# Performance work log

Measured on AMD Instinct MI355X. Metric: run time of the kernel, lower is better.

## Reference

```python
import jax, jax.numpy as jnp
import numpy as np

N = 100000   # nodes
E = 1600000  # edges (avg degree 16)
H = 8        # heads
C = 64       # per-head channels
G = 64       # graphs in batch
IN = 3       # input channels
OUT = 10     # classes
NEG_SLOPE = 0.2  # PyG GATConv default


def setup_inputs() -> dict:
    key = jax.random.key(0)
    ks = jax.random.split(key, 16)
    s = 0.1
    return {
        "x": jax.random.normal(ks[0], (N, IN), jnp.float32),
        "edge_index": jax.random.randint(ks[1], (2, E), 0, N),
        "batch": jnp.sort(jax.random.randint(ks[2], (N,), 0, G)),
        "W1": jax.random.normal(ks[3], (IN, H * C), jnp.float32) * s,
        "a1s": jax.random.normal(ks[4], (H, C), jnp.float32) * s,
        "a1d": jax.random.normal(ks[5], (H, C), jnp.float32) * s,
        "b1": jnp.zeros((H * C,), jnp.float32),
        "W2": jax.random.normal(ks[6], (H * C, H * C), jnp.float32) * s,
        "a2s": jax.random.normal(ks[7], (H, C), jnp.float32) * s,
        "a2d": jax.random.normal(ks[8], (H, C), jnp.float32) * s,
        "b2": jnp.zeros((H * C,), jnp.float32),
        "Wc": jax.random.normal(ks[9], (H * C, OUT), jnp.float32) * s,
        "bc": jnp.zeros((OUT,), jnp.float32),
    }


def _gat_layer(x, W, a_s, a_d, b, src, dst, n):
    # h: [N, H, C] per-head projected features
    h = (x @ W).reshape(n, H, C)
    # per-node attention logits per head
    al_s = jnp.einsum('nhc,hc->nh', h, a_s)
    al_d = jnp.einsum('nhc,hc->nh', h, a_d)
    # per-edge raw scores, [E', H]
    e = jax.nn.leaky_relu(al_s[src] + al_d[dst], NEG_SLOPE)
    # segment softmax over incoming edges of each destination node
    m = jax.ops.segment_max(e, dst, num_segments=n)
    ex = jnp.exp(e - m[dst])
    den = jax.ops.segment_sum(ex, dst, num_segments=n)
    alpha = ex / den[dst]  # [E', H]
    # weighted scatter-aggregate of source messages
    out = jax.ops.segment_sum(alpha[:, :, None] * h[src], dst, num_segments=n)
    return out.reshape(n, H * C) + b


def reference(x, edge_index, batch, W1, a1s, a1d, b1, W2, a2s, a2d, b2, Wc, bc):
    n = x.shape[0]
    ar = jnp.arange(n)
    # PyG GATConv adds self-loops by default
    src = jnp.concatenate([edge_index[0], ar])
    dst = jnp.concatenate([edge_index[1], ar])

    x1 = jax.nn.elu(_gat_layer(x, W1, a1s, a1d, b1, src, dst, n))
    x2 = jax.nn.elu(_gat_layer(x1, W2, a2s, a2d, b2, src, dst, n))

    # global mean pool over graphs
    sums = jax.ops.segment_sum(x2, batch, num_segments=G)
    cnt = jax.ops.segment_sum(jnp.ones((n, 1), x2.dtype), batch, num_segments=G)
    pooled = sums / jnp.maximum(cnt, 1.0)
    return pooled @ Wc + bc
```

## Files before the change

### kernel.cpp

```cpp
#include <hip/hip_runtime.h>
#include <math.h>

#define N_NODES 100000
#define N_EDGES 1600000
#define EP (N_EDGES + N_NODES)
#define NH 8
#define NC 64
#define NG 64
#define HC 512
#define SCAN_BLOCKS ((N_NODES + 255) / 256)
#define NPART 32
#define BPSTR 80

typedef unsigned short bf16_t;
typedef unsigned char fp8_t;
typedef __attribute__((ext_vector_type(8))) short short8;
typedef __attribute__((ext_vector_type(4))) float floatx4;
typedef __attribute__((ext_vector_type(2))) float floatx2;

__device__ inline float bf2f(bf16_t u) {
    union { unsigned int i; float f; } x;
    x.i = (unsigned int)u << 16;
    return x.f;
}
__device__ inline bf16_t f2bf(float f) {
    union { float f; unsigned int i; } x;
    x.f = f;
    unsigned int b = x.i;
    return (bf16_t)((b + 0x7fffu + ((b >> 16) & 1u)) >> 16);
}
__device__ inline fp8_t f2fp8(float f) {
    int v = __builtin_amdgcn_cvt_pk_fp8_f32(f, f, 0, false);
    return (fp8_t)v;
}

__device__ inline void ldsload16(const void* g, void* l) {
    __builtin_amdgcn_global_load_lds(
        (const __attribute__((address_space(1))) unsigned int*)g,
        (__attribute__((address_space(3))) unsigned int*)l, 16, 0, 0);
}

#define NBW2T (HC * HC / 256)
__global__ void k_prepw2t(const float* __restrict__ W1, const float* __restrict__ a1s,
                          const float* __restrict__ a1d, float* __restrict__ wprep,
                          const float* __restrict__ W2, bf16_t* __restrict__ W2T) {
    if (blockIdx.x == NBW2T) {
        int t = threadIdx.x;
        if (t < 48) {
            int isD = t >= 24;
            int tt = t % 24;
            int h = tt / 3, k = tt % 3;
            const float* a = isD ? a1d : a1s;
            float s = 0.f;
            for (int c = 0; c < 64; c++) s += W1[k * HC + h * 64 + c] * a[h * 64 + c];
            wprep[t] = s;
        }
        return;
    }
    int i = blockIdx.x * 256 + threadIdx.x;
    int n = i >> 9, kp = i & 511;
    int k = (kp & 7) * 64 + (kp >> 3);
    W2T[i] = f2bf(W2[k * HC + n]);
}

__global__ void k_deg(const int* __restrict__ ei, int* __restrict__ deg) {
    int i = blockIdx.x * 256 + threadIdx.x;
    if (i >= EP) return;
    int d = (i < N_EDGES) ? ei[N_EDGES + i] : (i - N_EDGES);
    atomicAdd(&deg[d], 1);
}

__global__ void k_scan1(const int* __restrict__ deg, int* __restrict__ rowptr, int* __restrict__ part) {
    __shared__ int s[256];
    int t = threadIdx.x, i = blockIdx.x * 256 + t;
    int v = (i < N_NODES) ? deg[i] : 0;
    s[t] = v;
    __syncthreads();
    for (int off = 1; off < 256; off <<= 1) {
        int u = (t >= off) ? s[t - off] : 0;
        __syncthreads();
        s[t] += u;
        __syncthreads();
    }
    if (i < N_NODES) rowptr[i] = s[t] - v;
    if (t == 255) part[blockIdx.x] = s[t];
}

__global__ void k_scan2(int* __restrict__ part, int* __restrict__ rowptr, int* __restrict__ gstart) {
    __shared__ int s[512];
    int t = threadIdx.x;
    int v = (t < SCAN_BLOCKS) ? part[t] : 0;
    s[t] = v;
    __syncthreads();
    for (int off = 1; off < 512; off <<= 1) {
        int u = (t >= off) ? s[t - off] : 0;
        __syncthreads();
        s[t] += u;
        __syncthreads();
    }
    part[t] = s[t] - v;
    if (t == 0) rowptr[N_NODES] = EP;
    if (t <= NG) gstart[t] = N_NODES;
}

__global__ void k_scan3(const int* __restrict__ part, int* __restrict__ rowptr,
                        int* __restrict__ cursor, const float* __restrict__ x,
                        bf16_t* __restrict__ xb, const int* __restrict__ batch,
                        int* __restrict__ gstart) {
    int i = blockIdx.x * 256 + threadIdx.x;
    if (i < N_NODES) {
        int v = rowptr[i] + part[blockIdx.x];
        rowptr[i] = v;
        cursor[i] = v;
        ushort4 p;
        p.x = f2bf(x[i * 3 + 0]);
        p.y = f2bf(x[i * 3 + 1]);
        p.z = f2bf(x[i * 3 + 2]);
        p.w = 0;
        *(ushort4*)&xb[i * 4] = p;
        int b = batch[i];
        if (i == 0) {
            for (int g = 0; g <= b; g++) gstart[g] = 0;
        } else {
            int bp = batch[i - 1];
            if (b != bp)
                for (int g = bp + 1; g <= b; g++) gstart[g] = i;
        }
    }
}

__global__ void k_scatter(const int* __restrict__ ei, int* __restrict__ cursor, int* __restrict__ csr) {
    int i = blockIdx.x * 256 + threadIdx.x;
    if (i >= EP) return;
    int s, d;
    if (i < N_EDGES) { s = ei[i]; d = ei[N_EDGES + i]; }
    else { s = i - N_EDGES; d = s; }
    int pos = atomicAdd(&cursor[d], 1);
    csr[pos] = s;
}

__global__ __launch_bounds__(64) void k_layer1(
    const bf16_t* __restrict__ xb, const int* __restrict__ rowptr, const int* __restrict__ csr,
    const float* __restrict__ W1, const float* __restrict__ wprep, const float* __restrict__ b1,
    bf16_t* __restrict__ x1p) {
    __shared__ float w1s[1536];
    __shared__ float wp[48];
    int lane = threadIdx.x;
#pragma unroll
    for (int q = 0; q < 6; q++)
        *(float4*)&w1s[(q * 64 + lane) * 4] = *(const float4*)&W1[(q * 64 + lane) * 4];
    if (lane < 48) wp[lane] = wprep[lane];
    __syncthreads();
    int half = lane >> 5, l32 = lane & 31;
    int dst = blockIdx.x * 2 + half;
    int rs = rowptr[dst], re = rowptr[dst + 1];
    ushort4 xd4 = *(const ushort4*)&xb[dst * 4];
    float xdx = bf2f(xd4.x), xdy = bf2f(xd4.y), xdz = bf2f(xd4.z);
    float ald[NH];
#pragma unroll
    for (int h = 0; h < NH; h++)
        ald[h] = xdx * wp[24 + h * 3] + xdy * wp[24 + h * 3 + 1] + xdz * wp[24 + h * 3 + 2];
    float den[NH], c0[NH], c1[NH], c2[NH];
#pragma unroll
    for (int h = 0; h < NH; h++) { den[h] = 0.f; c0[h] = 0.f; c1[h] = 0.f; c2[h] = 0.f; }
    for (int base = rs; base < re; base += 32) {
        int e = base + l32;
        if (e < re) {
            int s = csr[e];
            ushort4 sv4 = *(const ushort4*)&xb[s * 4];
            float svx = bf2f(sv4.x), svy = bf2f(sv4.y), svz = bf2f(sv4.z);
#pragma unroll
            for (int h = 0; h < NH; h++) {
                float ev = svx * wp[h * 3] + svy * wp[h * 3 + 1] + svz * wp[h * 3 + 2] + ald[h];
                ev = fmaxf(ev, 0.2f * ev);
                float w = __expf(ev);
                den[h] += w;
                c0[h] += w * svx;
                c1[h] += w * svy;
                c2[h] += w * svz;
            }
        }
    }
#pragma unroll
    for (int h = 0; h < NH; h++) {
#pragma unroll
        for (int off = 1; off < 32; off <<= 1) {
            den[h] += __shfl_xor(den[h], off, 64);
            c0[h] += __shfl_xor(c0[h], off, 64);
            c1[h] += __shfl_xor(c1[h], off, 64);
            c2[h] += __shfl_xor(c2[h], off, 64);
        }
    }
    bf16_t vbA[NH], vbB[NH];
#pragma unroll
    for (int h = 0; h < NH; h++) {
        int colA = h * 64 + l32;
        float vA = c0[h] * w1s[colA] + c1[h] * w1s[512 + colA] + c2[h] * w1s[1024 + colA];
        vA = vA / den[h] + b1[colA];
        vA = vA > 0.f ? vA : (__expf(vA) - 1.f);
        vbA[h] = f2bf(vA);
        int colB = colA + 32;
        float vB = c0[h] * w1s[colB] + c1[h] * w1s[512 + colB] + c2[h] * w1s[1024 + colB];
        vB = vB / den[h] + b1[colB];
        vB = vB > 0.f ? vB : (__expf(vB) - 1.f);
        vbB[h] = f2bf(vB);
    }
    uint4 oA, oB;
    oA.x = (unsigned int)vbA[0] | ((unsigned int)vbA[1] << 16);
    oA.y = (unsigned int)vbA[2] | ((unsigned int)vbA[3] << 16);
    oA.z = (unsigned int)vbA[4] | ((unsigned int)vbA[5] << 16);
    oA.w = (unsigned int)vbA[6] | ((unsigned int)vbA[7] << 16);
    oB.x = (unsigned int)vbB[0] | ((unsigned int)vbB[1] << 16);
    oB.y = (unsigned int)vbB[2] | ((unsigned int)vbB[3] << 16);
    oB.z = (unsigned int)vbB[4] | ((unsigned int)vbB[5] << 16);
    oB.w = (unsigned int)vbB[6] | ((unsigned int)vbB[7] << 16);
    *(uint4*)&x1p[(size_t)dst * HC + l32 * 8] = oA;
    *(uint4*)&x1p[(size_t)dst * HC + (l32 + 32) * 8] = oB;
}

__global__ __launch_bounds__(256) void k_gemm2(const bf16_t* __restrict__ A,
                                               const bf16_t* __restrict__ BT,
                                               fp8_t* __restrict__ Out,
                                               int row_base, int nrows,
                                               const float* __restrict__ a2s,
                                               const float* __restrict__ a2d,
                                               float* __restrict__ al2s,
                                               float* __restrict__ al2d) {
    __shared__ short smem[16384];
    short* As = smem;
    short* Bs = smem + 8192;
    int tid = threadIdx.x;
    int lane = tid & 63, wave = tid >> 6;
    int wm = wave & 1, wn = wave >> 1;
    int lm = lane & 15, quad = lane >> 4;
    int gx = blockIdx.x, gy = blockIdx.y;
    int l8 = lane >> 3, lc8 = lane & 7;
    int sw = lc8 ^ l8;
    const bf16_t* ga[4];
    const bf16_t* gb[4];
    short* la[4];
    short* lb[4];
#pragma unroll
    for (int it = 0; it < 4; it++) {
        int ar = gy * 128 + wave * 32 + it * 8 + l8;
        int arc = (ar < nrows) ? ar : 0;
        ga[it] = A + (size_t)(row_base + arc) * HC + sw * 8;
        gb[it] = BT + (size_t)(gx * 128 + wave * 32 + it * 8 + l8) * HC + sw * 8;
        la[it] = As + (wave * 32 + it * 8) * 64;
        lb[it] = Bs + (wave * 32 + it * 8) * 64;
    }

    floatx4 acc[4][4];
#pragma unroll
    for (int mi = 0; mi < 4; mi++)
#pragma unroll
        for (int ni = 0; ni < 4; ni++) acc[mi][ni] = (floatx4){0.f, 0.f, 0.f, 0.f};

    int lmw = lm & 7;
    for (int k0 = 0; k0 < HC; k0 += 64) {
        __syncthreads();
#pragma unroll
        for (int it = 0; it < 4; it++) ldsload16(ga[it] + k0, la[it]);
#pragma unroll
        for (int it = 0; it < 4; it++) ldsload16(gb[it] + k0, lb[it]);
        __syncthreads();
        short8 af[4][2], bf[4][2];
#pragma unroll
        for (int mi = 0; mi < 4; mi++)
#pragma unroll
            for (int kk = 0; kk < 2; kk++) {
                int pos = (kk * 4 + quad) ^ lmw;
                af[mi][kk] = *(const short8*)&As[(wm * 64 + mi * 16 + lm) * 64 + pos * 8];
            }
#pragma unroll
        for (int ni = 0; ni < 4; ni++)
#pragma unroll
            for (int kk = 0; kk < 2; kk++) {
                int pos = (kk * 4 + quad) ^ lmw;
                bf[ni][kk] = *(const short8*)&Bs[(wn * 64 + ni * 16 + lm) * 64 + pos * 8];
            }
#pragma unroll
        for (int mi = 0; mi < 4; mi++)
#pragma unroll
            for (int ni = 0; ni < 4; ni++) {
                acc[mi][ni] = __builtin_amdgcn_mfma_f32_16x16x32_bf16(af[mi][0], bf[ni][0], acc[mi][ni], 0, 0, 0);
                acc[mi][ni] = __builtin_amdgcn_mfma_f32_16x16x32_bf16(af[mi][1], bf[ni][1], acc[mi][ni], 0, 0, 0);
            }
    }
    int head = gx * 2 + wn;
    float a2sv[4], a2dv[4];
#pragma unroll
    for (int ni = 0; ni < 4; ni++) {
        int col = gx * 128 + wn * 64 + ni * 16 + lm;
        a2sv[ni] = a2s[col];
        a2dv[ni] = a2d[col];
    }
#pragma unroll
    for (int mi = 0; mi < 4; mi++) {
#pragma unroll
        for (int rg = 0; rg < 4; rg++) {
            int lrow = gy * 128 + wm * 64 + mi * 16 + quad * 4 + rg;
            float ps = 0.f, pd = 0.f;
#pragma unroll
            for (int ni = 0; ni < 4; ni++) {
                float v = acc[mi][ni][rg];
                ps += v * a2sv[ni];
                pd += v * a2dv[ni];
            }
#pragma unroll
            for (int off = 1; off < 16; off <<= 1) {
                ps += __shfl_xor(ps, off, 64);
                pd += __shfl_xor(pd, off, 64);
            }
            if (lrow < nrows && lm == 0) {
                int ar = row_base + lrow;
                al2s[ar * NH + head] = ps;
                al2d[ar * NH + head] = pd;
            }
        }
    }
    __syncthreads();
    unsigned char* bpatch = (unsigned char*)smem + wave * (32 * BPSTR);
#pragma unroll
    for (int p = 0; p < 2; p++) {
#pragma unroll
        for (int mih = 0; mih < 2; mih++) {
            int mi = p * 2 + mih;
#pragma unroll
            for (int ni = 0; ni < 4; ni++)
#pragma unroll
                for (int rg = 0; rg < 4; rg++) {
                    int rl = mih * 16 + quad * 4 + rg;
                    bpatch[rl * BPSTR + ni * 16 + lm] = f2fp8(acc[mi][ni][rg]);
                }
        }
#pragma unroll
        for (int it = 0; it < 2; it++) {
            int idx = it * 64 + lane;
            int rl = idx >> 2, c16 = idx & 3;
            uint4 v = *(uint4*)&bpatch[rl * BPSTR + c16 * 16];
            int lrow = gy * 128 + wm * 64 + p * 32 + rl;
            if (lrow < nrows)
                *(uint4*)&Out[(size_t)lrow * HC + wn * 64 + gx * 128 + c16 * 16] = v;
        }
        __syncthreads();
    }
}

#define ACC8(v, w) do { floatx2 c_;                                                            \
    c_ = __builtin_amdgcn_cvt_pk_f32_fp8((v).x, false); acc[0] += (w) * c_.x; acc[1] += (w) * c_.y; \
    c_ = __builtin_amdgcn_cvt_pk_f32_fp8((v).x, true);  acc[2] += (w) * c_.x; acc[3] += (w) * c_.y; \
    c_ = __builtin_amdgcn_cvt_pk_f32_fp8((v).y, false); acc[4] += (w) * c_.x; acc[5] += (w) * c_.y; \
    c_ = __builtin_amdgcn_cvt_pk_f32_fp8((v).y, true);  acc[6] += (w) * c_.x; acc[7] += (w) * c_.y; \
} while (0)

__global__ __launch_bounds__(64) void k_layer2pool(
    const fp8_t* __restrict__ h2lo, const fp8_t* __restrict__ h2hi, int srows,
    const float* __restrict__ al2s, const float* __restrict__ al2d,
    const int* __restrict__ rowptr, const int* __restrict__ csr, const float* __restrict__ b2,
    const int* __restrict__ batch, float* __restrict__ poolpart) {
    __shared__ float wlds[528];
    __shared__ int slds[64];
    int lane = threadIdx.x;
    int hme = lane >> 3;
    int hb = hme * 65;
    int dst = blockIdx.x;
    int rs = rowptr[dst], re = rowptr[dst + 1];
    float4 d0 = *(const float4*)&al2d[dst * NH];
    float4 d1 = *(const float4*)&al2d[dst * NH + 4];
    float ald[NH] = {d0.x, d0.y, d0.z, d0.w, d1.x, d1.y, d1.z, d1.w};
    float den[NH], acc[8];
#pragma unroll
    for (int h = 0; h < NH; h++) den[h] = 0.f;
#pragma unroll
    for (int q = 0; q < 8; q++) acc[q] = 0.f;
    for (int base = rs; base < re; base += 64) {
        int e = base + lane;
        int cl = re - base; if (cl > 64) cl = 64;
        float w[NH];
        int s = 0;
        if (e < re) {
            s = csr[e];
            float4 p0 = *(const float4*)&al2s[s * NH];
            float4 p1 = *(const float4*)&al2s[s * NH + 4];
            float als[NH] = {p0.x, p0.y, p0.z, p0.w, p1.x, p1.y, p1.z, p1.w};
#pragma unroll
            for (int h = 0; h < NH; h++) {
                float ev = als[h] + ald[h];
                ev = fmaxf(ev, 0.2f * ev);
                w[h] = __expf(ev);
                den[h] += w[h];
            }
        } else {
#pragma unroll
            for (int h = 0; h < NH; h++) w[h] = 0.f;
        }
        slds[lane] = s;
#pragma unroll
        for (int h = 0; h < NH; h++) wlds[h * 65 + lane] = w[h];
        int j = 0;
        for (; j + 7 < cl; j += 8) {
            uint2 vv[8]; float ww[8];
#pragma unroll
            for (int u = 0; u < 8; u++) {
                int s0 = slds[j + u];
                ww[u] = wlds[hb + j + u];
                const fp8_t* bp = (s0 < srows) ? (h2lo + (size_t)s0 * HC)
                                               : (h2hi + (size_t)(s0 - srows) * HC);
                vv[u] = *(const uint2*)&bp[lane * 8];
            }
#pragma unroll
            for (int u = 0; u < 8; u++) ACC8(vv[u], ww[u]);
        }
        if (j + 3 < cl) {
            uint2 vv[4]; float ww[4];
#pragma unroll
            for (int u = 0; u < 4; u++) {
                int s0 = slds[j + u];
                ww[u] = wlds[hb + j + u];
                const fp8_t* bp = (s0 < srows) ? (h2lo + (size_t)s0 * HC)
                                               : (h2hi + (size_t)(s0 - srows) * HC);
                vv[u] = *(const uint2*)&bp[lane * 8];
            }
#pragma unroll
            for (int u = 0; u < 4; u++) ACC8(vv[u], ww[u]);
            j += 4;
        }
        for (; j < cl; j++) {
            int sA = slds[j];
            float wA = wlds[hb + j];
            const fp8_t* bA = (sA < srows) ? (h2lo + (size_t)sA * HC)
                                           : (h2hi + (size_t)(sA - srows) * HC);
            uint2 vA = *(const uint2*)&bA[lane * 8];
            ACC8(vA, wA);
        }
    }
#pragma unroll
    for (int h = 0; h < NH; h++)
#pragma unroll
        for (int off = 1; off < 64; off <<= 1) den[h] += __shfl_xor(den[h], off, 64);
    float dd = den[0];
#pragma unroll
    for (int h = 1; h < NH; h++) dd = (hme == h) ? den[h] : dd;
    float dinv = 1.0f / dd;
    float4 ba = *(const float4*)&b2[lane * 8];
    float4 bb = *(const float4*)&b2[lane * 8 + 4];
    float bv[8] = {ba.x, ba.y, ba.z, ba.w, bb.x, bb.y, bb.z, bb.w};
#pragma unroll
    for (int q = 0; q < 8; q++) {
        float v = acc[q] * dinv + bv[q];
        v = v > 0.f ? v : (__expf(v) - 1.f);
        int c = lane * 8 + q;
        wlds[c + (c >> 5)] = v;
    }
    int g = batch[dst];
    float* pp = poolpart + ((size_t)(blockIdx.x & (NPART - 1)) * NG + g) * HC;
#pragma unroll
    for (int h = 0; h < NH; h++) {
        int c = h * 64 + lane;
        atomicAdd(&pp[c], wlds[c + (c >> 5)]);
    }
}

__global__ __launch_bounds__(256) void k_poolcls(const float* __restrict__ poolpart,
                                                 const int* __restrict__ gstart,
                                                 const float* __restrict__ Wc,
                                                 const float* __restrict__ bc,
                                                 float* __restrict__ out) {
    __shared__ float pl[512];
    int g = blockIdx.x, t = threadIdx.x;
    for (int c = t; c < HC; c += 256) {
        float s = 0.f;
        for (int p = 0; p < NPART; p++) s += poolpart[(size_t)p * NG * HC + g * HC + c];
        pl[c] = s;
    }
    __syncthreads();
    if (t < 10) {
        float cnt = fmaxf((float)(gstart[g + 1] - gstart[g]), 1.0f);
        float acc = 0.f;
        for (int k = 0; k < HC; k++) acc += pl[k] * Wc[k * 10 + t];
        out[g * 10 + t] = acc / cnt + bc[t];
    }
}

extern "C" void kernel_launch(void* const* d_in, const int* in_sizes, int n_in,
                              void* d_out, int out_size, void* d_ws, size_t ws_size,
                              hipStream_t stream) {
    const float* x   = (const float*)d_in[0];
    const int*   ei  = (const int*)d_in[1];
    const int*   bat = (const int*)d_in[2];
    const float* W1  = (const float*)d_in[3];
    const float* a1s = (const float*)d_in[4];
    const float* a1d = (const float*)d_in[5];
    const float* b1  = (const float*)d_in[6];
    const float* W2  = (const float*)d_in[7];
    const float* a2s = (const float*)d_in[8];
    const float* a2d = (const float*)d_in[9];
    const float* b2  = (const float*)d_in[10];
    const float* Wc  = (const float*)d_in[11];
    const float* bc  = (const float*)d_in[12];
    float* out = (float*)d_out;

    char* ws = (char*)d_ws;
    size_t off = 0;
    auto alloc = [&](size_t bytes) {
        size_t o = off;
        off += (bytes + 255) & ~(size_t)255;
        return o;
    };
    float*  wprep    = (float*)(ws + alloc(48 * 4));
    int*    rowptr   = (int*)(ws + alloc((size_t)(N_NODES + 1) * 4));
    int*    deg      = (int*)(ws + alloc((size_t)N_NODES * 4));
    int*    cursor   = (int*)(ws + alloc((size_t)N_NODES * 4));
    int*    part     = (int*)(ws + alloc(512 * 4));
    int*    gstart   = (int*)(ws + alloc(65 * 4));
    bf16_t* xb       = (bf16_t*)(ws + alloc((size_t)N_NODES * 4 * 2));
    int*    csr      = (int*)(ws + alloc((size_t)EP * 4));
    bf16_t* x1b      = (bf16_t*)(ws + alloc((size_t)N_NODES * HC * 2));
    float*  al2s     = (float*)(ws + alloc((size_t)N_NODES * NH * 4));
    float*  al2d     = (float*)(ws + alloc((size_t)N_NODES * NH * 4));
    float*  poolpart = (float*)(ws + alloc((size_t)NPART * NG * HC * 4));
    bf16_t* W2T = (bf16_t*)deg;

    size_t rem = (ws_size > off) ? ws_size - off : 0;
    int nslices, srows;
    if (rem >= (size_t)N_NODES * HC)      { nslices = 1;  srows = N_NODES; }
    else if (rem >= (size_t)50000 * HC)   { nslices = 2;  srows = 50000; }
    else if (rem >= (size_t)25000 * HC)   { nslices = 4;  srows = 25000; }
    else if (rem >= (size_t)12500 * HC)   { nslices = 8;  srows = 12500; }
    else                                  { nslices = 16; srows = 6250; }
    fp8_t* T = (fp8_t*)(ws + alloc((size_t)srows * HC));
    fp8_t* h2hi = (fp8_t*)x1b;

    hipMemsetAsync(deg, 0, (size_t)N_NODES * 4, stream);
    hipMemsetAsync(poolpart, 0, (size_t)NPART * NG * HC * 4, stream);

    k_deg<<<(EP + 255) / 256, 256, 0, stream>>>(ei, deg);
    k_scan1<<<SCAN_BLOCKS, 256, 0, stream>>>(deg, rowptr, part);
    k_scan2<<<1, 512, 0, stream>>>(part, rowptr, gstart);
    k_scan3<<<SCAN_BLOCKS, 256, 0, stream>>>(part, rowptr, cursor, x, xb, bat, gstart);
    k_scatter<<<(EP + 255) / 256, 256, 0, stream>>>(ei, cursor, csr);
    k_prepw2t<<<NBW2T + 1, 256, 0, stream>>>(W1, a1s, a1d, wprep, W2, W2T);
    k_layer1<<<N_NODES / 2, 64, 0, stream>>>(xb, rowptr, csr, W1, wprep, b1, x1b);
    for (int s = 0; s < nslices; s++) {
        fp8_t* outp = (s == 0) ? T : (h2hi + (size_t)(s - 1) * srows * HC);
        k_gemm2<<<dim3(4, (srows + 127) / 128), 256, 0, stream>>>(
            x1b, W2T, outp, s * srows, srows, a2s, a2d, al2s, al2d);
    }
    k_layer2pool<<<N_NODES, 64, 0, stream>>>(T, h2hi, srows, al2s, al2d,
                                             rowptr, csr, b2, bat, poolpart);
    k_poolcls<<<NG, 256, 0, stream>>>(poolpart, gstart, Wc, bc, out);
}
```

Baseline: 725.2 us.

## Process 16 destinations per block and pre-reduce pooling in LDS

The layer-2 aggregation+pool kernel now runs 256-thread blocks that each handle 16 consecutive destination nodes, four per wave. Because batch is sorted, each block's nodes map to at most a couple of graphs, so per-node outputs are summed in shared memory and flushed to global poolpart once per block rather than once per node. This cuts global atomic traffic by roughly 16x and reduces block launch count, at the cost of LDS atomics and a serial 4-node loop per wave that may lengthen tail latency on high-degree nodes.

```diff
diff --git a/kernel.cpp b/kernel.cpp
--- a/kernel.cpp
+++ b/kernel.cpp
@@ -11,6 +11,7 @@
 #define SCAN_BLOCKS ((N_NODES + 255) / 256)
 #define NPART 32
 #define BPSTR 80
+#define DPB 16
 
 typedef unsigned short bf16_t;
 typedef unsigned char fp8_t;
@@ -354,111 +355,136 @@
     c_ = __builtin_amdgcn_cvt_pk_f32_fp8((v).y, true);  acc[6] += (w) * c_.x; acc[7] += (w) * c_.y; \
 } while (0)
 
-__global__ __launch_bounds__(64) void k_layer2pool(
+__global__ __launch_bounds__(256) void k_layer2pool(
     const fp8_t* __restrict__ h2lo, const fp8_t* __restrict__ h2hi, int srows,
     const float* __restrict__ al2s, const float* __restrict__ al2d,
     const int* __restrict__ rowptr, const int* __restrict__ csr, const float* __restrict__ b2,
     const int* __restrict__ batch, float* __restrict__ poolpart) {
-    __shared__ float wlds[528];
-    __shared__ int slds[64];
-    int lane = threadIdx.x;
+    __shared__ float pacc[2][528];
+    __shared__ float wlds[4][528];
+    __shared__ int slds[4][64];
+    int tid = threadIdx.x;
+    int wave = tid >> 6, lane = tid & 63;
+    int base = blockIdx.x * DPB;
+    for (int c = tid; c < 1056; c += 256) ((float*)pacc)[c] = 0.f;
+    int g0 = batch[base];
+    int g1 = batch[base + DPB - 1];
+    __syncthreads();
     int hme = lane >> 3;
     int hb = hme * 65;
-    int dst = blockIdx.x;
-    int rs = rowptr[dst], re = rowptr[dst + 1];
-    float4 d0 = *(const float4*)&al2d[dst * NH];
-    float4 d1 = *(const float4*)&al2d[dst * NH + 4];
-    float ald[NH] = {d0.x, d0.y, d0.z, d0.w, d1.x, d1.y, d1.z, d1.w};
-    float den[NH], acc[8];
-#pragma unroll
-    for (int h = 0; h < NH; h++) den[h] = 0.f;
-#pragma unroll
-    for (int q = 0; q < 8; q++) acc[q] = 0.f;
-    for (int base = rs; base < re; base += 64) {
-        int e = base + lane;
-        int cl = re - base; if (cl > 64) cl = 64;
-        float w[NH];
-        int s = 0;
-        if (e < re) {
-            s = csr[e];
-            float4 p0 = *(const float4*)&al2s[s * NH];
-            float4 p1 = *(const float4*)&al2s[s * NH + 4];
-            float als[NH] = {p0.x, p0.y, p0.z, p0.w, p1.x, p1.y, p1.z, p1.w};
-#pragma unroll
-            for (int h = 0; h < NH; h++) {
-                float ev = als[h] + ald[h];
-                ev = fmaxf(ev, 0.2f * ev);
-                w[h] = __expf(ev);
-                den[h] += w[h];
-            }
-        } else {
-#pragma unroll
-            for (int h = 0; h < NH; h++) w[h] = 0.f;
-        }
-        slds[lane] = s;
-#pragma unroll
-        for (int h = 0; h < NH; h++) wlds[h * 65 + lane] = w[h];
-        int j = 0;
-        for (; j + 7 < cl; j += 8) {
-            uint2 vv[8]; float ww[8];
-#pragma unroll
-            for (int u = 0; u < 8; u++) {
-                int s0 = slds[j + u];
-                ww[u] = wlds[hb + j + u];
-                const fp8_t* bp = (s0 < srows) ? (h2lo + (size_t)s0 * HC)
-                                               : (h2hi + (size_t)(s0 - srows) * HC);
-                vv[u] = *(const uint2*)&bp[lane * 8];
-            }
-#pragma unroll
-            for (int u = 0; u < 8; u++) ACC8(vv[u], ww[u]);
-        }
-        if (j + 3 < cl) {
-            uint2 vv[4]; float ww[4];
-#pragma unroll
-            for (int u = 0; u < 4; u++) {
-                int s0 = slds[j + u];
-                ww[u] = wlds[hb + j + u];
-                const fp8_t* bp = (s0 < srows) ? (h2lo + (size_t)s0 * HC)
-                                               : (h2hi + (size_t)(s0 - srows) * HC);
-                vv[u] = *(const uint2*)&bp[lane * 8];
-            }
-#pragma unroll
-            for (int u = 0; u < 4; u++) ACC8(vv[u], ww[u]);
-            j += 4;
-        }
-        for (; j < cl; j++) {
-            int sA = slds[j];
-            float wA = wlds[hb + j];
-            const fp8_t* bA = (sA < srows) ? (h2lo + (size_t)sA * HC)
-                                           : (h2hi + (size_t)(sA - srows) * HC);
-            uint2 vA = *(const uint2*)&bA[lane * 8];
-            ACC8(vA, wA);
-        }
-    }
-#pragma unroll
-    for (int h = 0; h < NH; h++)
-#pragma unroll
-        for (int off = 1; off < 64; off <<= 1) den[h] += __shfl_xor(den[h], off, 64);
-    float dd = den[0];
-#pragma unroll
-    for (int h = 1; h < NH; h++) dd = (hme == h) ? den[h] : dd;
-    float dinv = 1.0f / dd;
     float4 ba = *(const float4*)&b2[lane * 8];
     float4 bb = *(const float4*)&b2[lane * 8 + 4];
     float bv[8] = {ba.x, ba.y, ba.z, ba.w, bb.x, bb.y, bb.z, bb.w};
-#pragma unroll
-    for (int q = 0; q < 8; q++) {
-        float v = acc[q] * dinv + bv[q];
-        v = v > 0.f ? v : (__expf(v) - 1.f);
-        int c = lane * 8 + q;
-        wlds[c + (c >> 5)] = v;
-    }
-    int g = batch[dst];
-    float* pp = poolpart + ((size_t)(blockIdx.x & (NPART - 1)) * NG + g) * HC;
-#pragma unroll
-    for (int h = 0; h < NH; h++) {
-        int c = h * 64 + lane;
-        atomicAdd(&pp[c], wlds[c + (c >> 5)]);
+    float* mywlds = wlds[wave];
+    int* myslds = slds[wave];
+    for (int di = 0; di < 4; di++) {
+        int dst = base + wave * 4 + di;
+        int rs = rowptr[dst], re = rowptr[dst + 1];
+        float4 d0 = *(const float4*)&al2d[dst * NH];
+        float4 d1 = *(const float4*)&al2d[dst * NH + 4];
+        float ald[NH] = {d0.x, d0.y, d0.z, d0.w, d1.x, d1.y, d1.z, d1.w};
+        float den[NH], acc[8];
+#pragma unroll
+        for (int h = 0; h < NH; h++) den[h] = 0.f;
+#pragma unroll
+        for (int q = 0; q < 8; q++) acc[q] = 0.f;
+        for (int eb = rs; eb < re; eb += 64) {
+            int e = eb + lane;
+            int cl = re - eb; if (cl > 64) cl = 64;
+            float w[NH];
+            int s = 0;
+            if (e < re) {
+                s = csr[e];
+                float4 p0 = *(const float4*)&al2s[s * NH];
+                float4 p1 = *(const float4*)&al2s[s * NH + 4];
+                float als[NH] = {p0.x, p0.y, p0.z, p0.w, p1.x, p1.y, p1.z, p1.w};
+#pragma unroll
+                for (int h = 0; h < NH; h++) {
+                    float ev = als[h] + ald[h];
+                    ev = fmaxf(ev, 0.2f * ev);
+                    w[h] = __expf(ev);
+                    den[h] += w[h];
+                }
+            } else {
+#pragma unroll
+                for (int h = 0; h < NH; h++) w[h] = 0.f;
+            }
+            myslds[lane] = s;
+#pragma unroll
+            for (int h = 0; h < NH; h++) mywlds[h * 65 + lane] = w[h];
+            int j = 0;
+            for (; j + 7 < cl; j += 8) {
+                uint2 vv[8]; float ww[8];
+#pragma unroll
+                for (int u = 0; u < 8; u++) {
+                    int s0 = myslds[j + u];
+                    ww[u] = mywlds[hb + j + u];
+                    const fp8_t* bp = (s0 < srows) ? (h2lo + (size_t)s0 * HC)
+                                                   : (h2hi + (size_t)(s0 - srows) * HC);
+                    vv[u] = *(const uint2*)&bp[lane * 8];
+                }
+#pragma unroll
+                for (int u = 0; u < 8; u++) ACC8(vv[u], ww[u]);
+            }
+            if (j + 3 < cl) {
+                uint2 vv[4]; float ww[4];
+#pragma unroll
+                for (int u = 0; u < 4; u++) {
+                    int s0 = myslds[j + u];
+                    ww[u] = mywlds[hb + j + u];
+                    const fp8_t* bp = (s0 < srows) ? (h2lo + (size_t)s0 * HC)
+                                                   : (h2hi + (size_t)(s0 - srows) * HC);
+                    vv[u] = *(const uint2*)&bp[lane * 8];
+                }
+#pragma unroll
+                for (int u = 0; u < 4; u++) ACC8(vv[u], ww[u]);
+                j += 4;
+            }
+            for (; j < cl; j++) {
+                int sA = myslds[j];
+                float wA = mywlds[hb + j];
+                const fp8_t* bA = (sA < srows) ? (h2lo + (size_t)sA * HC)
+                                               : (h2hi + (size_t)(sA - srows) * HC);
+                uint2 vA = *(const uint2*)&bA[lane * 8];
+                ACC8(vA, wA);
+            }
+        }
+#pragma unroll
+        for (int h = 0; h < NH; h++)
+#pragma unroll
+            for (int off = 1; off < 64; off <<= 1) den[h] += __shfl_xor(den[h], off, 64);
+        float dd = den[0];
+#pragma unroll
+        for (int h = 1; h < NH; h++) dd = (hme == h) ? den[h] : dd;
+        float dinv = 1.0f / dd;
+        int g = batch[dst];
+        if (g == g0 || g == g1) {
+            float* pa = pacc[(g == g0) ? 0 : 1];
+#pragma unroll
+            for (int q = 0; q < 8; q++) {
+                float v = acc[q] * dinv + bv[q];
+                v = v > 0.f ? v : (__expf(v) - 1.f);
+                int c = lane * 8 + q;
+                atomicAdd(&pa[c + (c >> 5)], v);
+            }
+        } else {
+            float* pp = poolpart + ((size_t)(blockIdx.x & (NPART - 1)) * NG + g) * HC;
+#pragma unroll
+            for (int q = 0; q < 8; q++) {
+                float v = acc[q] * dinv + bv[q];
+                v = v > 0.f ? v : (__expf(v) - 1.f);
+                atomicAdd(&pp[lane * 8 + q], v);
+            }
+        }
+    }
+    __syncthreads();
+    float* pp0 = poolpart + ((size_t)(blockIdx.x & (NPART - 1)) * NG + g0) * HC;
+    for (int c = tid; c < HC; c += 256)
+        atomicAdd(&pp0[c], pacc[0][c + (c >> 5)]);
+    if (g1 != g0) {
+        float* pp1 = poolpart + ((size_t)(blockIdx.x & (NPART - 1)) * NG + g1) * HC;
+        for (int c = tid; c < HC; c += 256)
+            atomicAdd(&pp1[c], pacc[1][c + (c >> 5)]);
     }
 }
 
@@ -547,7 +573,7 @@
         k_gemm2<<<dim3(4, (srows + 127) / 128), 256, 0, stream>>>(
             x1b, W2T, outp, s * srows, srows, a2s, a2d, al2s, al2d);
     }
-    k_layer2pool<<<N_NODES, 64, 0, stream>>>(T, h2hi, srows, al2s, al2d,
-                                             rowptr, csr, b2, bat, poolpart);
+    k_layer2pool<<<N_NODES / DPB, 256, 0, stream>>>(T, h2hi, srows, al2s, al2d,
+                                                    rowptr, csr, b2, bat, poolpart);
     k_poolcls<<<NG, 256, 0, stream>>>(poolpart, gstart, Wc, bc, out);
 }
```

Result: slower. 845.9 us (+16.6%).
